# Optimization experiments

Measured on AMD Instinct MI355X. Metric: run time of the kernel, lower is better.

Reference implementation:

```python
import jax, jax.numpy as jnp
import numpy as np

N, T, D = 128, 2048, 88

def setup_inputs() -> dict:
    key = jax.random.key(0)
    k1, k2 = jax.random.split(key)
    output = jax.random.normal(k1, (N, T, D), dtype=jnp.float32)
    # binary piano-roll style target (sparse note activations)
    target = (jax.random.uniform(k2, (N, T, D)) < 0.1).astype(jnp.float32)
    mask = jnp.ones((N, T), dtype=jnp.int32)  # left-aligned valid mask
    return {"output": output, "target": target, "mask": mask}

def reference(output, target, mask):
    # prediction = (sigmoid(output) > 0.5) -> non-differentiable 0/1 floats
    pred = (jax.nn.sigmoid(output) > 0.5).astype(output.dtype)
    # tru_pos summed over both feature and time dims -> [N]
    tru_pos = jnp.sum(pred * target, axis=(1, 2))
    # per-timestep false pos / false neg -> [N, T]
    false_pos = jnp.sum(pred * (1.0 - target), axis=2)
    false_neg = jnp.sum((1.0 - pred) * target, axis=2)
    # T_i = number of valid timesteps per sequence (loop runs over t < T_i)
    T_i = jnp.sum(mask, axis=1)  # [N] int
    valid = (jnp.arange(false_pos.shape[1])[None, :] < T_i[:, None]).astype(output.dtype)
    ratio = tru_pos[:, None] / (tru_pos[:, None] + false_pos + false_neg)  # [N, T]
    acc = jnp.sum(ratio * valid, axis=1) / T_i.astype(output.dtype)  # [N]
    return jnp.sum(acc)
```

## Files before the change

kernel.cpp:

```cpp
#include <hip/hip_runtime.h>
#include <stdint.h>

#define NN 128
#define TT 2048
#define DD 88
#define ROWS 32
#define F4_ROW 22
#define F4_TILE (ROWS * F4_ROW)
#define INSTR_PER_ARR 11
#define K1_BLOCKS (NN * TT / ROWS)
#define PARTS_PER_N (TT / ROWS)

typedef float f4 __attribute__((ext_vector_type(4)));
typedef const __attribute__((address_space(1))) uint32_t guint;
typedef __attribute__((address_space(3))) uint32_t luint;

__global__ __launch_bounds__(256) void acc_rowstats_kernel(
    const float* __restrict__ outp, const float* __restrict__ tgt,
    float* __restrict__ fpfn, float* __restrict__ tp_part) {
  __shared__ f4 lds_o[F4_TILE];
  __shared__ f4 lds_g[F4_TILE];
  __shared__ float s_tp[4];

  const int tid = threadIdx.x;
  const int lane = tid & 63;
  const int wave = tid >> 6;
  const int blk = blockIdx.x;
  const size_t tile_f = (size_t)blk * (ROWS * DD);

  for (int j = wave; j < 2 * INSTR_PER_ARR; j += 4) {
    const int is_g = (j >= INSTR_PER_ARR) ? 1 : 0;
    const int idx = j - is_g * INSTR_PER_ARR;
    const float* src = (is_g ? tgt : outp) + tile_f + idx * 256;
    float* dst = (is_g ? (float*)lds_g : (float*)lds_o) + idx * 256;
    __builtin_amdgcn_global_load_lds((guint*)src + lane * 4, (luint*)dst,
                                     16, 0, 0);
  }
  __syncthreads();

  const int r = tid >> 3;
  const int s = tid & 7;
  float tp = 0.f;
  float x = 0.f;
#pragma unroll
  for (int j0 = 0; j0 < 3; ++j0) {
    const int j = s + j0 * 8;
    if (j < F4_ROW) {
      const f4 o = lds_o[r * F4_ROW + j];
      const f4 g = lds_g[r * F4_ROW + j];
      {
        const float pf = (o.x > 0.f) ? 1.f : 0.f;
        x += fabsf(pf - g.x);
        tp = fmaf(pf, g.x, tp);
      }
      {
        const float pf = (o.y > 0.f) ? 1.f : 0.f;
        x += fabsf(pf - g.y);
        tp = fmaf(pf, g.y, tp);
      }
      {
        const float pf = (o.z > 0.f) ? 1.f : 0.f;
        x += fabsf(pf - g.z);
        tp = fmaf(pf, g.z, tp);
      }
      {
        const float pf = (o.w > 0.f) ? 1.f : 0.f;
        x += fabsf(pf - g.w);
        tp = fmaf(pf, g.w, tp);
      }
    }
  }
  x += __shfl_down(x, 4, 64);
  x += __shfl_down(x, 2, 64);
  x += __shfl_down(x, 1, 64);
  if (s == 0) fpfn[(size_t)blk * ROWS + r] = x;

  for (int off = 32; off > 0; off >>= 1) tp += __shfl_down(tp, off, 64);
  if (lane == 0) s_tp[wave] = tp;
  __syncthreads();
  if (tid == 0) tp_part[blk] = s_tp[0] + s_tp[1] + s_tp[2] + s_tp[3];
}

__global__ __launch_bounds__(256) void acc_finalize_kernel(
    const int* __restrict__ mask, const float* __restrict__ fpfn,
    const float* __restrict__ tp_part, float* __restrict__ out) {
  const int n = blockIdx.x;
  const int tid = threadIdx.x;
  __shared__ float sa[256], sb[256];

  const int4* m4 = (const int4*)(mask + (size_t)n * TT);
  int ti = 0;
#pragma unroll
  for (int it = 0; it < 2; ++it) {
    const int4 v = m4[it * 256 + tid];
    ti += v.x + v.y + v.z + v.w;
  }
  const float tpv = (tid < PARTS_PER_N) ? tp_part[n * PARTS_PER_N + tid] : 0.f;

  sa[tid] = (float)ti;
  sb[tid] = tpv;
  __syncthreads();
  for (int s = 128; s > 0; s >>= 1) {
    if (tid < s) { sa[tid] += sa[tid + s]; sb[tid] += sb[tid + s]; }
    __syncthreads();
  }
  const float fTi = sa[0];
  const float tp = sb[0];
  const int Ti = (int)fTi;
  __syncthreads();

  const float* __restrict__ fr = fpfn + (size_t)n * TT;
  float a = 0.f;
  for (int t = tid; t < Ti; t += 256) a += tp / (tp + fr[t]);
  sa[tid] = a;
  __syncthreads();
  for (int s = 128; s > 0; s >>= 1) {
    if (tid < s) sa[tid] += sa[tid + s];
    __syncthreads();
  }
  if (tid == 0) atomicAdd(out, sa[0] / fTi);
}

extern "C" void kernel_launch(void* const* d_in, const int* in_sizes, int n_in,
                              void* d_out, int out_size, void* d_ws, size_t ws_size,
                              hipStream_t stream) {
  const float* output = (const float*)d_in[0];
  const float* target = (const float*)d_in[1];
  const int* mask = (const int*)d_in[2];
  float* out = (float*)d_out;

  float* tp_part = (float*)d_ws;
  float* fpfn = tp_part + K1_BLOCKS;

  hipMemsetAsync(d_out, 0, sizeof(float) * out_size, stream);
  acc_rowstats_kernel<<<K1_BLOCKS, 256, 0, stream>>>(output, target, fpfn, tp_part);
  acc_finalize_kernel<<<NN, 256, 0, stream>>>(mask, fpfn, tp_part, out);
}
```

Measured before the change: 204.2 us.

## Split finalize into per-chunk blocks plus single-block sum, drop memset

The per-sequence finalize kernel (128 blocks) is replaced by 1024 blocks that each handle one 256-timestep chunk, with wave-shuffle reductions instead of LDS tree reductions. A third single-block kernel sums the chunk results, which removes the memset and the atomicAdd. The aim is to fill more of the GPU in the tail phase and cut synchronization steps, at the cost of one extra kernel launch and each chunk block re-reading the full mask row and the tp partials.

```diff
diff --git a/kernel.cpp b/kernel.cpp
--- a/kernel.cpp
+++ b/kernel.cpp
@@ -10,6 +10,8 @@
 #define INSTR_PER_ARR 11
 #define K1_BLOCKS (NN * TT / ROWS)
 #define PARTS_PER_N (TT / ROWS)
+#define CPN 8
+#define K2_BLOCKS (NN * CPN)
 
 typedef float f4 __attribute__((ext_vector_type(4)));
 typedef const __attribute__((address_space(1))) uint32_t guint;
@@ -81,44 +83,57 @@
   if (tid == 0) tp_part[blk] = s_tp[0] + s_tp[1] + s_tp[2] + s_tp[3];
 }
 
-__global__ __launch_bounds__(256) void acc_finalize_kernel(
+__global__ __launch_bounds__(256) void acc_chunk_kernel(
     const int* __restrict__ mask, const float* __restrict__ fpfn,
-    const float* __restrict__ tp_part, float* __restrict__ out) {
-  const int n = blockIdx.x;
+    const float* __restrict__ tp_part, float* __restrict__ accp) {
+  const int b = blockIdx.x;
+  const int n = b >> 3;
+  const int c = b & (CPN - 1);
   const int tid = threadIdx.x;
-  __shared__ float sa[256], sb[256];
+  const int lane = tid & 63;
+  const int wave = tid >> 6;
+  __shared__ float s_ti[4];
+  __shared__ float s_tp[4];
+  __shared__ float s_a[4];
 
   const int4* m4 = (const int4*)(mask + (size_t)n * TT);
-  int ti = 0;
-#pragma unroll
-  for (int it = 0; it < 2; ++it) {
-    const int4 v = m4[it * 256 + tid];
-    ti += v.x + v.y + v.z + v.w;
+  const int4 v0 = m4[tid];
+  const int4 v1 = m4[tid + 256];
+  const float tpv = (tid < PARTS_PER_N) ? tp_part[n * PARTS_PER_N + tid] : 0.f;
+  const int t = c * 256 + tid;
+  const float fr = fpfn[(size_t)n * TT + t];
+
+  int ti = v0.x + v0.y + v0.z + v0.w + v1.x + v1.y + v1.z + v1.w;
+  float tp = tpv;
+  for (int off = 32; off > 0; off >>= 1) {
+    ti += __shfl_down(ti, off, 64);
+    tp += __shfl_down(tp, off, 64);
   }
-  const float tpv = (tid < PARTS_PER_N) ? tp_part[n * PARTS_PER_N + tid] : 0.f;
+  if (lane == 0) { s_ti[wave] = (float)ti; s_tp[wave] = tp; }
+  __syncthreads();
+  const float fTi = s_ti[0] + s_ti[1] + s_ti[2] + s_ti[3];
+  const float tpn = s_tp[0] + s_tp[1] + s_tp[2] + s_tp[3];
+  const int Ti = (int)fTi;
 
-  sa[tid] = (float)ti;
-  sb[tid] = tpv;
+  float a = (t < Ti) ? tpn / (tpn + fr) : 0.f;
+  for (int off = 32; off > 0; off >>= 1) a += __shfl_down(a, off, 64);
+  if (lane == 0) s_a[wave] = a;
   __syncthreads();
-  for (int s = 128; s > 0; s >>= 1) {
-    if (tid < s) { sa[tid] += sa[tid + s]; sb[tid] += sb[tid + s]; }
-    __syncthreads();
-  }
-  const float fTi = sa[0];
-  const float tp = sb[0];
-  const int Ti = (int)fTi;
+  if (tid == 0)
+    accp[b] = (s_a[0] + s_a[1] + s_a[2] + s_a[3]) / fTi;
+}
+
+__global__ __launch_bounds__(256) void acc_sum_kernel(
+    const float* __restrict__ accp, float* __restrict__ out) {
+  const int tid = threadIdx.x;
+  const int lane = tid & 63;
+  const int wave = tid >> 6;
+  __shared__ float s_a[4];
+  float a = accp[tid] + accp[tid + 256] + accp[tid + 512] + accp[tid + 768];
+  for (int off = 32; off > 0; off >>= 1) a += __shfl_down(a, off, 64);
+  if (lane == 0) s_a[wave] = a;
   __syncthreads();
-
-  const float* __restrict__ fr = fpfn + (size_t)n * TT;
-  float a = 0.f;
-  for (int t = tid; t < Ti; t += 256) a += tp / (tp + fr[t]);
-  sa[tid] = a;
-  __syncthreads();
-  for (int s = 128; s > 0; s >>= 1) {
-    if (tid < s) sa[tid] += sa[tid + s];
-    __syncthreads();
-  }
-  if (tid == 0) atomicAdd(out, sa[0] / fTi);
+  if (tid == 0) out[0] = s_a[0] + s_a[1] + s_a[2] + s_a[3];
 }
 
 extern "C" void kernel_launch(void* const* d_in, const int* in_sizes, int n_in,
@@ -131,8 +146,9 @@
 
   float* tp_part = (float*)d_ws;
   float* fpfn = tp_part + K1_BLOCKS;
+  float* accp = fpfn + (size_t)NN * TT;
 
-  hipMemsetAsync(d_out, 0, sizeof(float) * out_size, stream);
   acc_rowstats_kernel<<<K1_BLOCKS, 256, 0, stream>>>(output, target, fpfn, tp_part);
-  acc_finalize_kernel<<<NN, 256, 0, stream>>>(mask, fpfn, tp_part, out);
+  acc_chunk_kernel<<<K2_BLOCKS, 256, 0, stream>>>(mask, fpfn, tp_part, accp);
+  acc_sum_kernel<<<1, 256, 0, stream>>>(accp, out);
 }
```

Measured after the change: 199.8 us, median of 2. 2.2% less time.
